# Kernel tuning notes

Hardware: AMD Instinct MI355X
Metric: run time of the kernel (lower is better)

## Reference

```python
import jax, jax.numpy as jnp
import numpy as np

B, N, E, T, S = 4096, 16, 512, 128, 256  # batch, num_experts, expert_dim, task_dim, scenario_dim


def setup_inputs() -> dict:
    key = jax.random.key(0)
    k1, k2, k3, k4 = jax.random.split(key, 4)
    return {
        "scene_repr": jax.random.normal(k1, (B, S), dtype=jnp.float32),
        "task_anchor": jax.random.normal(k2, (B, T), dtype=jnp.float32),
        "expert_reprs": jax.random.normal(k3, (B, N, E), dtype=jnp.float32),
        "v": jax.random.normal(k4, (E + T, 1), dtype=jnp.float32),
    }


def reference(scene_repr, task_anchor, expert_reprs, v):
    # Original: score_i = concat([expert_i, task_anchor]) @ v for each expert i.
    # Vectorized: split v into expert part and task part; task contribution is
    # identical for every expert, so compute it once and broadcast.
    E_ = expert_reprs.shape[-1]
    v_e = v[:E_, 0]   # [E]
    v_t = v[E_:, 0]   # [T]
    scores = jnp.einsum('bne,e->bn', expert_reprs, v_e) + (task_anchor @ v_t)[:, None]  # [B, N]
    attention_weights = jax.nn.softmax(scores, axis=1)  # [B, N]
    aggregated_repr = jnp.einsum('bne,bn->be', expert_reprs, attention_weights)  # [B, E]
    return aggregated_repr, attention_weights
```

## Files before the change

kernel.cpp:

```cpp
#include <hip/hip_runtime.h>


#define NB 4096
#define NEXP 16
#define EDIM 512

typedef float f32x2 __attribute__((ext_vector_type(2)));
typedef float f32x4 __attribute__((ext_vector_type(4)));

__global__ __launch_bounds__(256, 4) void meta_attn_kernel(
    const float* __restrict__ expert,
    const float* __restrict__ v,
    float* __restrict__ out_agg,
    float* __restrict__ out_w)
{
    const int wave = threadIdx.x >> 6;
    const int lane = threadIdx.x & 63;
    const int b = blockIdx.x;

    const int eoff = 128 * wave + 2 * lane;
    const float* row = expert + (size_t)b * (NEXP * EDIM) + eoff;

    const f32x2 ve = *(const f32x2*)(v + eoff);

    f32x2 tile[NEXP];
#pragma unroll
    for (int n = 0; n < NEXP; ++n)
        tile[n] = *(const f32x2*)(row + n * EDIM);

    float cur[NEXP];
#pragma unroll
    for (int n = 0; n < NEXP; ++n)
        cur[n] = tile[n].x * ve.x + tile[n].y * ve.y;

    float t8[8];
    {
        const bool hi = (lane & 1) != 0;
#pragma unroll
        for (int j = 0; j < 8; ++j) {
            const float send = hi ? cur[j] : cur[j + 8];
            const float keep = hi ? cur[j + 8] : cur[j];
            t8[j] = keep + __shfl_xor(send, 1, 64);
        }
    }
    float t4[4];
    {
        const bool hi = (lane & 2) != 0;
#pragma unroll
        for (int j = 0; j < 4; ++j) {
            const float send = hi ? t8[j] : t8[j + 4];
            const float keep = hi ? t8[j + 4] : t8[j];
            t4[j] = keep + __shfl_xor(send, 2, 64);
        }
    }
    float t2[2];
    {
        const bool hi = (lane & 4) != 0;
#pragma unroll
        for (int j = 0; j < 2; ++j) {
            const float send = hi ? t2[j] - t2[j] + t4[j] : t4[j + 2];
            (void)send;
        }
#pragma unroll
        for (int j = 0; j < 2; ++j) {
            const float send2 = hi ? t4[j] : t4[j + 2];
            const float keep2 = hi ? t4[j + 2] : t4[j];
            t2[j] = keep2 + __shfl_xor(send2, 4, 64);
        }
    }
    float t1;
    {
        const bool hi = (lane & 8) != 0;
        const float send = hi ? t2[0] : t2[1];
        const float keep = hi ? t2[1] : t2[0];
        t1 = keep + __shfl_xor(send, 8, 64);
    }
    t1 += __shfl_xor(t1, 16, 64);
    t1 += __shfl_xor(t1, 32, 64);

    __shared__ float lds_s[NEXP][4];
    if (lane < 16) {
        const int idx = ((lane & 1) << 3) | ((lane & 2) << 1) |
                        ((lane & 4) >> 1) | ((lane & 8) >> 3);
        lds_s[idx][wave] = t1;
    }
    __syncthreads();

    float s[NEXP];
#pragma unroll
    for (int n = 0; n < NEXP; ++n) {
        const f32x4 p = *(const f32x4*)(&lds_s[n][0]);
        s[n] = (p.x + p.y) + (p.z + p.w);
    }

    float mx = s[0];
#pragma unroll
    for (int n = 1; n < NEXP; ++n) mx = fmaxf(mx, s[n]);
    float w[NEXP];
    float sum = 0.0f;
#pragma unroll
    for (int n = 0; n < NEXP; ++n) {
        w[n] = __expf(s[n] - mx);
        sum += w[n];
    }
    const float inv = 1.0f / sum;
#pragma unroll
    for (int n = 0; n < NEXP; ++n) w[n] *= inv;

    f32x2 acc = {0.f, 0.f};
#pragma unroll
    for (int n = 0; n < NEXP; ++n) {
        acc.x += w[n] * tile[n].x;
        acc.y += w[n] * tile[n].y;
    }
    *(f32x2*)(out_agg + (size_t)b * EDIM + eoff) = acc;

    if (wave == 0) {
        float myw = w[0];
#pragma unroll
        for (int n = 1; n < NEXP; ++n) myw = (lane == n) ? w[n] : myw;
        if (lane < NEXP) out_w[(size_t)b * NEXP + lane] = myw;
    }
}

extern "C" void kernel_launch(void* const* d_in, const int* in_sizes, int n_in,
                              void* d_out, int out_size, void* d_ws, size_t ws_size,
                              hipStream_t stream) {
    const float* expert = (const float*)d_in[2];
    const float* v      = (const float*)d_in[3];
    float* out_agg = (float*)d_out;
    float* out_w   = (float*)d_out + (size_t)NB * EDIM;

    meta_attn_kernel<<<dim3(NB), dim3(256), 0, stream>>>(expert, v, out_agg, out_w);
}
```

Measured before the change: 26.39 us.

## Stage expert tile into LDS via direct global_load_lds instead of registers

Replaces per-thread strided register loads of the 16x512 expert tile with contiguous 16-byte global-to-LDS DMA loads (global_load_lds), then reads the tile from shared memory for both the scoring and the aggregation passes. The aim is fully coalesced, wide global transfers and less register pressure. The cost is 32KB of LDS per block, which limits occupancy, plus an extra barrier and extra LDS reads. Some dead code in the shuffle reduction is also cleaned up.

```diff
diff --git a/kernel.cpp b/kernel.cpp
--- a/kernel.cpp
+++ b/kernel.cpp
@@ -6,7 +6,6 @@
 #define EDIM 512
 
 typedef float f32x2 __attribute__((ext_vector_type(2)));
-typedef float f32x4 __attribute__((ext_vector_type(4)));
 
 __global__ __launch_bounds__(256, 4) void meta_attn_kernel(
     const float* __restrict__ expert,
@@ -18,20 +17,32 @@
     const int lane = threadIdx.x & 63;
     const int b = blockIdx.x;
 
+    __shared__ float smem[NEXP * EDIM];
+    __shared__ float lds_s[NEXP][4];
+
+    {
+        const float* gbase = expert + (size_t)b * (NEXP * EDIM) + wave * 2048;
+        float* lbase = smem + wave * 2048;
+#pragma unroll
+        for (int i = 0; i < 8; ++i) {
+            __builtin_amdgcn_global_load_lds(
+                (const __attribute__((address_space(1))) void*)(gbase + i * 256 + lane * 4),
+                (__attribute__((address_space(3))) void*)(lbase + i * 256),
+                16, 0, 0);
+        }
+    }
+
     const int eoff = 128 * wave + 2 * lane;
-    const float* row = expert + (size_t)b * (NEXP * EDIM) + eoff;
-
     const f32x2 ve = *(const f32x2*)(v + eoff);
 
-    f32x2 tile[NEXP];
-#pragma unroll
-    for (int n = 0; n < NEXP; ++n)
-        tile[n] = *(const f32x2*)(row + n * EDIM);
+    __syncthreads();
 
     float cur[NEXP];
 #pragma unroll
-    for (int n = 0; n < NEXP; ++n)
-        cur[n] = tile[n].x * ve.x + tile[n].y * ve.y;
+    for (int n = 0; n < NEXP; ++n) {
+        const f32x2 t = *(const f32x2*)(&smem[n * EDIM + eoff]);
+        cur[n] = t.x * ve.x + t.y * ve.y;
+    }
 
     float t8[8];
     {
@@ -58,14 +69,9 @@
         const bool hi = (lane & 4) != 0;
 #pragma unroll
         for (int j = 0; j < 2; ++j) {
-            const float send = hi ? t2[j] - t2[j] + t4[j] : t4[j + 2];
-            (void)send;
-        }
-#pragma unroll
-        for (int j = 0; j < 2; ++j) {
-            const float send2 = hi ? t4[j] : t4[j + 2];
-            const float keep2 = hi ? t4[j + 2] : t4[j];
-            t2[j] = keep2 + __shfl_xor(send2, 4, 64);
+            const float send = hi ? t4[j] : t4[j + 2];
+            const float keep = hi ? t4[j + 2] : t4[j];
+            t2[j] = keep + __shfl_xor(send, 4, 64);
         }
     }
     float t1;
@@ -78,7 +84,6 @@
     t1 += __shfl_xor(t1, 16, 64);
     t1 += __shfl_xor(t1, 32, 64);
 
-    __shared__ float lds_s[NEXP][4];
     if (lane < 16) {
         const int idx = ((lane & 1) << 3) | ((lane & 2) << 1) |
                         ((lane & 4) >> 1) | ((lane & 8) >> 3);
@@ -88,10 +93,8 @@
 
     float s[NEXP];
 #pragma unroll
-    for (int n = 0; n < NEXP; ++n) {
-        const f32x4 p = *(const f32x4*)(&lds_s[n][0]);
-        s[n] = (p.x + p.y) + (p.z + p.w);
-    }
+    for (int n = 0; n < NEXP; ++n)
+        s[n] = (lds_s[n][0] + lds_s[n][1]) + (lds_s[n][2] + lds_s[n][3]);
 
     float mx = s[0];
 #pragma unroll
@@ -110,8 +113,9 @@
     f32x2 acc = {0.f, 0.f};
 #pragma unroll
     for (int n = 0; n < NEXP; ++n) {
-        acc.x += w[n] * tile[n].x;
-        acc.y += w[n] * tile[n].y;
+        const f32x2 t = *(const f32x2*)(&smem[n * EDIM + eoff]);
+        acc.x += w[n] * t.x;
+        acc.y += w[n] * t.y;
     }
     *(f32x2*)(out_agg + (size_t)b * EDIM + eoff) = acc;
 
```

After: 27.38 us. +3.7%, slower.
